# Kernel optimization log

Hardware: AMD Instinct MI355X
Metric: run time of the kernel (lower is better)

## Reference

```python
import jax, jax.numpy as jnp
import numpy as np

H = 1024
S = 65536


def setup_inputs() -> dict:
    key = jax.random.key(0)
    k1, k2, k3, k4 = jax.random.split(key, 4)
    hidden = jax.random.normal(k1, (H,), dtype=jnp.float32)
    encoder_outputs = jax.random.normal(k2, (S, H), dtype=jnp.float32)
    # nn.Linear(H, H) params, scaled like PyTorch default init (~1/sqrt(H))
    W = jax.random.normal(k3, (H, H), dtype=jnp.float32) / np.sqrt(H)
    b = jax.random.normal(k4, (H,), dtype=jnp.float32) / np.sqrt(H)
    return {"hidden": hidden, "encoder_outputs": encoder_outputs, "W": W, "b": b}


def reference(hidden, encoder_outputs, W, b):
    # Original per-timestep loop: scores[i] = hidden . (W @ enc[i] + b)
    # Fused batched form: enc @ (W^T @ hidden) + (b . hidden)  -- same math,
    # one streaming GEMV over the [S, H] encoder outputs instead of S launches.
    v = W.T @ hidden                      # [H]
    scores = encoder_outputs @ v + jnp.dot(b, hidden)  # [S]
    attn = jax.nn.softmax(scores)         # softmax over seq dim
    return attn[None, None, :]            # [1, 1, S]
```

## Files before the change

### kernel.cpp

```cpp
#include <hip/hip_runtime.h>

#define H 1024
#define S 65536

typedef float vfloat4 __attribute__((ext_vector_type(4)));

__global__ __launch_bounds__(256) void k1a_partial(const float* __restrict__ W,
                                                   const float* __restrict__ hidden,
                                                   float* __restrict__ partial) {
    const int t = threadIdx.x;
    const int b = blockIdx.x;
    const int i0 = b * 8;
    vfloat4 acc = (vfloat4)(0.f);
    #pragma unroll
    for (int r = 0; r < 8; ++r) {
        const float hv = hidden[i0 + r];
        const vfloat4 w = *(const vfloat4*)(W + (size_t)(i0 + r) * H + t * 4);
        acc += w * hv;
    }
    *(vfloat4*)(partial + (size_t)b * H + t * 4) = acc;
}

__global__ __launch_bounds__(256) void k1b_reduce(const float* __restrict__ partial,
                                                  float* __restrict__ v) {
    const int j = blockIdx.x * 256 + threadIdx.x;
    float s0 = 0.f, s1 = 0.f;
    for (int b = 0; b < 128; b += 2) {
        s0 += partial[(size_t)b * H + j];
        s1 += partial[(size_t)(b + 1) * H + j];
    }
    v[j] = s0 + s1;
}

__global__ __launch_bounds__(256) void k_scores(const float* __restrict__ enc,
                                                const float* __restrict__ v,
                                                float* __restrict__ scores,
                                                float* __restrict__ bmax,
                                                float* __restrict__ bsum) {
    const int lane = threadIdx.x & 63;
    const int warp = threadIdx.x >> 6;
    const vfloat4 vr0 = *(const vfloat4*)(v + lane * 4);
    const vfloat4 vr1 = *(const vfloat4*)(v + 256 + lane * 4);
    const vfloat4 vr2 = *(const vfloat4*)(v + 512 + lane * 4);
    const vfloat4 vr3 = *(const vfloat4*)(v + 768 + lane * 4);

    const int wg = blockIdx.x * 4 + warp;
    float m = -INFINITY;
    float s = 0.f;

    #pragma unroll
    for (int it = 0; it < 4; ++it) {
        const int r0 = wg * 2 + it * 16384;
        const int r1 = r0 + 1;
        const float* e0 = enc + (size_t)r0 * H;
        const float* e1 = enc + (size_t)r1 * H;
        const vfloat4 a0 = *(const vfloat4*)(e0 + lane * 4);
        const vfloat4 a1 = *(const vfloat4*)(e0 + 256 + lane * 4);
        const vfloat4 a2 = *(const vfloat4*)(e0 + 512 + lane * 4);
        const vfloat4 a3 = *(const vfloat4*)(e0 + 768 + lane * 4);
        const vfloat4 b0 = *(const vfloat4*)(e1 + lane * 4);
        const vfloat4 b1 = *(const vfloat4*)(e1 + 256 + lane * 4);
        const vfloat4 b2 = *(const vfloat4*)(e1 + 512 + lane * 4);
        const vfloat4 b3 = *(const vfloat4*)(e1 + 768 + lane * 4);
        const vfloat4 p0 = a0 * vr0 + a1 * vr1 + a2 * vr2 + a3 * vr3;
        const vfloat4 p1 = b0 * vr0 + b1 * vr1 + b2 * vr2 + b3 * vr3;
        float acc0 = (p0.x + p0.y) + (p0.z + p0.w);
        float acc1 = (p1.x + p1.y) + (p1.z + p1.w);
        const float t0 = __shfl_xor(acc0, 32, 64);
        const float t1 = __shfl_xor(acc1, 32, 64);
        float c = (lane < 32) ? (acc0 + t0) : (acc1 + t1);
        #pragma unroll
        for (int mm = 1; mm < 32; mm <<= 1) c += __shfl_xor(c, mm, 64);
        if (lane == 0)  scores[r0] = c;
        if (lane == 32) scores[r1] = c;
        const float mn = fmaxf(m, c);
        s = s * __expf(m - mn) + __expf(c - mn);
        m = mn;
    }
    const float mo = __shfl_xor(m, 32, 64);
    const float so = __shfl_xor(s, 32, 64);
    const float mm2 = fmaxf(m, mo);
    s = s * __expf(m - mm2) + so * __expf(mo - mm2);
    m = mm2;

    __shared__ float smx[4], ssm[4];
    if (lane == 0) { smx[warp] = m; ssm[warp] = s; }
    __syncthreads();
    if (threadIdx.x == 0) {
        const float M = fmaxf(fmaxf(smx[0], smx[1]), fmaxf(smx[2], smx[3]));
        const float SS = ssm[0] * __expf(smx[0] - M) + ssm[1] * __expf(smx[1] - M)
                       + ssm[2] * __expf(smx[2] - M) + ssm[3] * __expf(smx[3] - M);
        bmax[blockIdx.x] = M;
        bsum[blockIdx.x] = SS;
    }
}

__global__ __launch_bounds__(256) void k_final(const float* __restrict__ scores,
                                               const float* __restrict__ bmax,
                                               const float* __restrict__ bsum,
                                               float* __restrict__ out) {
    const int t = threadIdx.x;
    const int lane = t & 63;
    const int warp = t >> 6;

    float lm[8];
    float m = -INFINITY;
    #pragma unroll
    for (int k = 0; k < 8; ++k) {
        lm[k] = bmax[t + k * 256];
        m = fmaxf(m, lm[k]);
    }
    #pragma unroll
    for (int d = 1; d < 64; d <<= 1) m = fmaxf(m, __shfl_xor(m, d, 64));
    __shared__ float sm[4];
    if (lane == 0) sm[warp] = m;
    __syncthreads();
    const float gmax = fmaxf(fmaxf(sm[0], sm[1]), fmaxf(sm[2], sm[3]));

    float p = 0.f;
    #pragma unroll
    for (int k = 0; k < 8; ++k) p += bsum[t + k * 256] * __expf(lm[k] - gmax);
    #pragma unroll
    for (int d = 1; d < 64; d <<= 1) p += __shfl_xor(p, d, 64);
    __shared__ float sp[4];
    if (lane == 0) sp[warp] = p;
    __syncthreads();
    const float inv = 1.0f / ((sp[0] + sp[1]) + (sp[2] + sp[3]));

    const int i = blockIdx.x * 256 + t;
    out[i] = __expf(scores[i] - gmax) * inv;
}

extern "C" void kernel_launch(void* const* d_in, const int* in_sizes, int n_in,
                              void* d_out, int out_size, void* d_ws, size_t ws_size,
                              hipStream_t stream) {
    const float* hidden = (const float*)d_in[0];
    const float* enc    = (const float*)d_in[1];
    const float* W      = (const float*)d_in[2];
    float* out = (float*)d_out;

    float* v       = (float*)d_ws;
    float* scores  = v + 1024;
    float* bmax    = scores + S;
    float* bsum    = bmax + 2048;
    float* partial = bsum + 2048;

    k1a_partial<<<128,  256, 0, stream>>>(W, hidden, partial);
    k1b_reduce <<<4,    256, 0, stream>>>(partial, v);
    k_scores   <<<2048, 256, 0, stream>>>(enc, v, scores, bmax, bsum);
    k_final    <<<256,  256, 0, stream>>>(scores, bmax, bsum, out);
}
```

Measured before the change: 387.4 us.

## Double-buffer encoder row loads with nontemporal loads and halve score grid

The scores kernel now handles 8 row pairs per wave instead of 4 and runs on half as many blocks. Loads are software-pipelined across two register buffers so the next pair's loads are in flight while the current pair is reduced. Encoder and W reads use nontemporal loads to avoid polluting cache with streamed data. The final kernel and workspace layout are resized to match 1024 partial blocks. This raises register use and lowers the number of resident waves, which trades occupancy for more memory-level parallelism per wave.

```diff
diff --git a/kernel.cpp b/kernel.cpp
--- a/kernel.cpp
+++ b/kernel.cpp
@@ -4,6 +4,10 @@
 #define S 65536
 
 typedef float vfloat4 __attribute__((ext_vector_type(4)));
+
+__device__ __forceinline__ vfloat4 nt_load4(const float* p) {
+    return __builtin_nontemporal_load((const vfloat4*)p);
+}
 
 __global__ __launch_bounds__(256) void k1a_partial(const float* __restrict__ W,
                                                    const float* __restrict__ hidden,
@@ -15,7 +19,7 @@
     #pragma unroll
     for (int r = 0; r < 8; ++r) {
         const float hv = hidden[i0 + r];
-        const vfloat4 w = *(const vfloat4*)(W + (size_t)(i0 + r) * H + t * 4);
+        const vfloat4 w = nt_load4(W + (size_t)(i0 + r) * H + t * 4);
         acc += w * hv;
     }
     *(vfloat4*)(partial + (size_t)b * H + t * 4) = acc;
@@ -45,38 +49,61 @@
     const vfloat4 vr3 = *(const vfloat4*)(v + 768 + lane * 4);
 
     const int wg = blockIdx.x * 4 + warp;
+    const float* base = enc + (size_t)(wg * 2) * H + lane * 4;
+
     float m = -INFINITY;
     float s = 0.f;
 
-    #pragma unroll
-    for (int it = 0; it < 4; ++it) {
-        const int r0 = wg * 2 + it * 16384;
-        const int r1 = r0 + 1;
-        const float* e0 = enc + (size_t)r0 * H;
-        const float* e1 = enc + (size_t)r1 * H;
-        const vfloat4 a0 = *(const vfloat4*)(e0 + lane * 4);
-        const vfloat4 a1 = *(const vfloat4*)(e0 + 256 + lane * 4);
-        const vfloat4 a2 = *(const vfloat4*)(e0 + 512 + lane * 4);
-        const vfloat4 a3 = *(const vfloat4*)(e0 + 768 + lane * 4);
-        const vfloat4 b0 = *(const vfloat4*)(e1 + lane * 4);
-        const vfloat4 b1 = *(const vfloat4*)(e1 + 256 + lane * 4);
-        const vfloat4 b2 = *(const vfloat4*)(e1 + 512 + lane * 4);
-        const vfloat4 b3 = *(const vfloat4*)(e1 + 768 + lane * 4);
-        const vfloat4 p0 = a0 * vr0 + a1 * vr1 + a2 * vr2 + a3 * vr3;
-        const vfloat4 p1 = b0 * vr0 + b1 * vr1 + b2 * vr2 + b3 * vr3;
-        float acc0 = (p0.x + p0.y) + (p0.z + p0.w);
-        float acc1 = (p1.x + p1.y) + (p1.z + p1.w);
-        const float t0 = __shfl_xor(acc0, 32, 64);
-        const float t1 = __shfl_xor(acc1, 32, 64);
-        float c = (lane < 32) ? (acc0 + t0) : (acc1 + t1);
-        #pragma unroll
-        for (int mm = 1; mm < 32; mm <<= 1) c += __shfl_xor(c, mm, 64);
-        if (lane == 0)  scores[r0] = c;
-        if (lane == 32) scores[r1] = c;
-        const float mn = fmaxf(m, c);
-        s = s * __expf(m - mn) + __expf(c - mn);
-        m = mn;
-    }
+    vfloat4 A0, A1, A2, A3, A4, A5, A6, A7;
+    vfloat4 B0, B1, B2, B3, B4, B5, B6, B7;
+
+#define LOADB(P, IT) do { \
+    const float* _p = base + (size_t)(IT) * 8192 * H; \
+    P##0 = nt_load4(_p);        P##1 = nt_load4(_p + 256); \
+    P##2 = nt_load4(_p + 512);  P##3 = nt_load4(_p + 768); \
+    P##4 = nt_load4(_p + 1024); P##5 = nt_load4(_p + 1280); \
+    P##6 = nt_load4(_p + 1536); P##7 = nt_load4(_p + 1792); \
+} while (0)
+
+#define COMP(P, IT) do { \
+    const vfloat4 p0 = P##0 * vr0 + P##1 * vr1 + P##2 * vr2 + P##3 * vr3; \
+    const vfloat4 p1 = P##4 * vr0 + P##5 * vr1 + P##6 * vr2 + P##7 * vr3; \
+    float acc0 = (p0.x + p0.y) + (p0.z + p0.w); \
+    float acc1 = (p1.x + p1.y) + (p1.z + p1.w); \
+    const float t0 = __shfl_xor(acc0, 32, 64); \
+    const float t1 = __shfl_xor(acc1, 32, 64); \
+    float c = (lane < 32) ? (acc0 + t0) : (acc1 + t1); \
+    c += __shfl_xor(c, 1, 64);  c += __shfl_xor(c, 2, 64); \
+    c += __shfl_xor(c, 4, 64);  c += __shfl_xor(c, 8, 64); \
+    c += __shfl_xor(c, 16, 64); \
+    const int _r0 = wg * 2 + (IT) * 8192; \
+    if (lane == 0)  scores[_r0] = c; \
+    if (lane == 32) scores[_r0 + 1] = c; \
+    const float _mn = fmaxf(m, c); \
+    s = s * __expf(m - _mn) + __expf(c - _mn); \
+    m = _mn; \
+} while (0)
+
+    LOADB(A, 0);
+    LOADB(B, 1);
+    COMP(A, 0);
+    LOADB(A, 2);
+    COMP(B, 1);
+    LOADB(B, 3);
+    COMP(A, 2);
+    LOADB(A, 4);
+    COMP(B, 3);
+    LOADB(B, 5);
+    COMP(A, 4);
+    LOADB(A, 6);
+    COMP(B, 5);
+    LOADB(B, 7);
+    COMP(A, 6);
+    COMP(B, 7);
+
+#undef LOADB
+#undef COMP
+
     const float mo = __shfl_xor(m, 32, 64);
     const float so = __shfl_xor(s, 32, 64);
     const float mm2 = fmaxf(m, mo);
@@ -103,10 +130,10 @@
     const int lane = t & 63;
     const int warp = t >> 6;
 
-    float lm[8];
+    float lm[4];
     float m = -INFINITY;
     #pragma unroll
-    for (int k = 0; k < 8; ++k) {
+    for (int k = 0; k < 4; ++k) {
         lm[k] = bmax[t + k * 256];
         m = fmaxf(m, lm[k]);
     }
@@ -119,7 +146,7 @@
 
     float p = 0.f;
     #pragma unroll
-    for (int k = 0; k < 8; ++k) p += bsum[t + k * 256] * __expf(lm[k] - gmax);
+    for (int k = 0; k < 4; ++k) p += bsum[t + k * 256] * __expf(lm[k] - gmax);
     #pragma unroll
     for (int d = 1; d < 64; d <<= 1) p += __shfl_xor(p, d, 64);
     __shared__ float sp[4];
@@ -142,11 +169,11 @@
     float* v       = (float*)d_ws;
     float* scores  = v + 1024;
     float* bmax    = scores + S;
-    float* bsum    = bmax + 2048;
-    float* partial = bsum + 2048;
+    float* bsum    = bmax + 1024;
+    float* partial = bsum + 1024;
 
     k1a_partial<<<128,  256, 0, stream>>>(W, hidden, partial);
     k1b_reduce <<<4,    256, 0, stream>>>(partial, v);
-    k_scores   <<<2048, 256, 0, stream>>>(enc, v, scores, bmax, bsum);
+    k_scores   <<<1024, 256, 0, stream>>>(enc, v, scores, bmax, bsum);
     k_final    <<<256,  256, 0, stream>>>(scores, bmax, bsum, out);
 }
```

Measured after the change: 360.7 us. 6.9% less time.
